# Kernel optimization log

Hardware: AMD Instinct MI355X
Metric: run time of the kernel (lower is better)

The kernel has to match this reference:

```python
import jax, jax.numpy as jnp
import numpy as np

N, V, NF, EF, EMB, OUT, MP = 512, 40, 32, 4, 128, 128, 3
BIG_NEG = -1.0e6


def _build_graph():
    """Build a batch of random molecule-like graphs (path + extra edges, one-hot
    bond features) and replicate the torch index-construction logic in numpy."""
    rng = np.random.default_rng(0)
    edges = np.zeros((N, V, V, EF), np.float32)
    perm = np.argsort(rng.random((N, V)), axis=1)
    b = np.repeat(np.arange(N), V - 1)
    i = perm[:, :-1].ravel(); j = perm[:, 1:].ravel()
    t = rng.integers(0, EF, b.shape)
    edges[b, i, j, t] = 1.0; edges[b, j, i, t] = 1.0
    NEX = 6  # extra edges per graph
    u = rng.integers(0, V, (N, NEX))
    v = rng.integers(0, V - 1, (N, NEX)); v = v + (v >= u)  # no self loops
    b2 = np.repeat(np.arange(N), NEX); t2 = rng.integers(0, EF, b2.shape)
    edges[b2, u.ravel(), v.ravel(), t2] = 1.0; edges[b2, v.ravel(), u.ravel(), t2] = 1.0
    # keep edge features strictly one-hot (adjacency = edges.sum(-1) must be 0/1)
    multi = edges.sum(-1) > 1
    edges = np.where(multi[..., None], np.eye(EF, dtype=np.float32)[edges.argmax(-1)], edges)

    adj = (edges.sum(-1) > 0).astype(np.float32)            # (N,V,V) binary
    b_idx, n_idx, nb_idx = np.nonzero(adj)                  # directed edge list, row-major
    E = b_idx.shape[0]
    adj_e = np.zeros((N, V, V), np.int64)
    adj_e[b_idx, n_idx, nb_idx] = np.arange(1, E + 1)       # edge-id+1 in adjacency slots
    rows = adj_e[b_idx, nb_idx, :]                          # (E,V): edges into each edge's nghb
    deg = (rows > 0).sum(1)
    eb = rows[rows > 0] - 1                                 # ingoing edge ids (row-major = torch cat order)
    igeb = np.repeat(np.arange(E), deg)                     # receiving-edge index
    ige = np.arange(deg.sum()) - np.repeat(np.cumsum(deg) - deg, deg)  # slot within receiver
    keep = n_idx[igeb] != nb_idx[eb]                        # drop the reverse edge
    eb, igeb, ige = eb[keep], igeb[keep], ige[keep]
    D = int(adj.sum(-1).max())                              # max node degree
    mask = np.zeros((E, D), np.float32); mask[igeb, ige] = 1.0
    node_mask = (adj.sum(-1) > 0).astype(np.float32)        # (N,V)
    return edges, b_idx, n_idx, nb_idx, eb, igeb, ige, mask, node_mask


def setup_inputs() -> dict:
    edges, b_idx, n_idx, nb_idx, eb, igeb, ige, mask, node_mask = _build_graph()
    key = jax.random.key(0)
    ks = jax.random.split(key, 8)
    def lin(k, fi, fo):
        return (jax.random.normal(k, (fi, fo), jnp.float32) / np.sqrt(fi)).astype(jnp.float32)
    return dict(
        nodes=jax.random.normal(ks[0], (N, V, NF), jnp.float32),
        edges=jnp.asarray(edges),
        W_pre=lin(ks[1], 2 * NF + EF, EMB), b_pre=jnp.zeros((EMB,), jnp.float32),
        W_att=lin(ks[2], 2 * EMB, EMB), b_att=jnp.zeros((EMB,), jnp.float32),
        W_emb=lin(ks[3], 2 * EMB, EMB), b_emb=jnp.zeros((EMB,), jnp.float32),
        Wg_att=lin(ks[4], 2 * EMB, EMB), bg_att=jnp.zeros((EMB,), jnp.float32),
        Wg_emb=lin(ks[5], EMB, EMB), bg_emb=jnp.zeros((EMB,), jnp.float32),
        W_out=lin(ks[6], EMB, OUT), b_out=jnp.zeros((OUT,), jnp.float32),
        ingoing_mask=jnp.asarray(mask), node_mask=jnp.asarray(node_mask),
        eb_b=jnp.asarray(b_idx, jnp.int32), eb_n=jnp.asarray(n_idx, jnp.int32),
        eb_nb=jnp.asarray(nb_idx, jnp.int32),
        in_eb=jnp.asarray(eb, jnp.int32), in_igeb=jnp.asarray(igeb, jnp.int32),
        in_ige=jnp.asarray(ige, jnp.int32),
    )


def reference(nodes, edges, W_pre, b_pre, W_att, b_att, W_emb, b_emb,
              Wg_att, bg_att, Wg_emb, bg_emb, W_out, b_out,
              ingoing_mask, node_mask, eb_b, eb_n, eb_nb, in_eb, in_igeb, in_ige):
    E, D = ingoing_mask.shape
    # preprocess_edges (EMN): tanh MLP on [node, neighbour, edge] per directed edge
    e_in = jnp.concatenate([nodes[eb_b, eb_n], nodes[eb_b, eb_nb],
                            edges[eb_b, eb_n, eb_nb]], axis=-1)        # (E, 2NF+EF)
    e_emb = jnp.tanh(e_in @ W_pre + b_pre)                              # (E, EMB)
    energy_mask = (1.0 - ingoing_mask)[:, :, None] * BIG_NEG            # (E, D, 1)
    e_bcast = jnp.broadcast_to(e_emb[:, None, :], (E, D, EMB))

    def step(mem, _):
        # scatter ingoing edge memories into padded (E, D, EMB) slots, then
        # attention-aggregate (propagate_edges of EMN)
        in_mem = jnp.zeros((E, D, EMB), mem.dtype).at[in_igeb, in_ige].set(mem[in_eb])
        cat = jnp.concatenate([e_bcast, in_mem], axis=-1)               # (E, D, 2EMB)
        att = jax.nn.softmax(cat @ W_att + b_att + energy_mask, axis=1)
        msg = jnp.tanh(cat @ W_emb + b_emb)
        return (att * msg).sum(1), None

    mem0 = jnp.zeros((E, EMB), nodes.dtype)
    mem, _ = jax.lax.scan(step, mem0, None, length=MP)                  # (E, EMB)
    # node_sets scatter + sum over degree slots == segment-sum per (graph, node)
    graph_sets = jax.ops.segment_sum(mem, eb_b * V + eb_n,
                                     num_segments=N * V).reshape(N, V, EMB)
    # readout: attention GraphGather + dense head
    cat3 = jnp.concatenate([graph_sets, graph_sets], axis=-1)           # hidden == input
    g_att = jax.nn.softmax(cat3 @ Wg_att + bg_att +
                           (1.0 - node_mask)[:, :, None] * BIG_NEG, axis=1)
    g_emb = jnp.tanh(graph_sets @ Wg_emb + bg_emb)
    graph_embedding = (g_att * g_emb).sum(1)                            # (N, EMB)
    return graph_embedding @ W_out + b_out                              # (N, OUT)
```

## Files before the change

### kernel.cpp

```cpp
#include <hip/hip_runtime.h>
#include <hip/hip_bf16.h>
#include <math.h>

#define NN 512
#define VN 40
#define NF 32
#define EFD 4
#define OUTD 128
#define EMAX 96
#define DMAX 8
#define MSTR 136
#define WPSTR 104
#define NT 1024
#define NW 16

typedef __attribute__((ext_vector_type(8))) short short8;
typedef __attribute__((ext_vector_type(4))) float f32x4;

__device__ __forceinline__ float fast_tanh(float x) {
    return fmaf(-2.0f, __builtin_amdgcn_rcpf(__expf(2.0f * x) + 1.0f), 1.0f);
}

__global__ __launch_bounds__(256) void k_setup(
    const int* __restrict__ igeb, const int* __restrict__ eb_b,
    const float* __restrict__ W_att, const float* __restrict__ W_emb,
    const float* __restrict__ Wg_att, const float* __restrict__ Wg_emb,
    const float* __restrict__ W_pre,
    int* __restrict__ off, int* __restrict__ eoff,
    __hip_bfloat16* __restrict__ Wt1, __hip_bfloat16* __restrict__ Wt2,
    __hip_bfloat16* __restrict__ Wt3, __hip_bfloat16* __restrict__ Wpt,
    int K, int E, int nbO, int nbK)
{
    int bid = blockIdx.x, tid = threadIdx.x;
    if (bid < nbO) {
        int e = bid * 256 + tid;
        if (e >= E) return;
        int b = eb_b[e];
        if (e == 0) { for (int bb = 0; bb <= b; ++bb) off[bb] = 0; }
        else { int pb = eb_b[e - 1]; for (int bb = pb + 1; bb <= b; ++bb) off[bb] = e; }
        if (e == E - 1) { for (int bb = b + 1; bb <= NN; ++bb) off[bb] = E; }
        return;
    }
    bid -= nbO;
    if (bid < nbK) {
        int k = bid * 256 + tid;
        if (k >= K) return;
        int e = igeb[k];
        if (k == 0) { for (int ee = 0; ee <= e; ++ee) eoff[ee] = 0; }
        else { int pe = igeb[k - 1]; for (int ee = pe + 1; ee <= e; ++ee) eoff[ee] = k; }
        if (k == K - 1) { for (int ee = e + 1; ee <= E; ++ee) eoff[ee] = K; }
        return;
    }
    bid -= nbK;
    int c = bid * 2 + (tid >> 7), k = tid & 127;
    int cc = c & 127; bool hi = c >= 128;
    if (!hi) {
        Wt1[c * 128 + k] = __float2bfloat16(W_emb[k * 128 + c]);
        if (k < WPSTR)
            Wpt[c * WPSTR + k] = __float2bfloat16(k < 68 ? W_pre[k * 128 + c] : 0.f);
    }
    Wt2[c * 128 + k] = __float2bfloat16(hi ? W_emb[(128 + k) * 128 + cc] : W_att[(128 + k) * 128 + cc]);
    Wt3[c * 128 + k] = __float2bfloat16(hi ? Wg_emb[k * 128 + cc]
                                           : (Wg_att[k * 128 + cc] + Wg_att[(128 + k) * 128 + cc]));
}

__global__ __launch_bounds__(256) void k_pre2(
    const float* __restrict__ nodes, const float* __restrict__ edges,
    const __hip_bfloat16* __restrict__ Wpt, const float* __restrict__ b_pre,
    const int* __restrict__ eb_b, const int* __restrict__ eb_n, const int* __restrict__ eb_nb,
    const __hip_bfloat16* __restrict__ Wt1, const float* __restrict__ b_emb,
    __hip_bfloat16* __restrict__ beB, int E)
{
    __shared__ __align__(16) __hip_bfloat16 eIn[64 * WPSTR];
    __shared__ __align__(16) __hip_bfloat16 eL[64 * MSTR];
    __shared__ int bL[64], nL[64], nbL[64];
    int tid = threadIdx.x;
    int e0 = blockIdx.x * 64;
    if (tid < 64) {
        int e = e0 + tid;
        int b = -1, n = 0, nb = 0;
        if (e < E) { b = eb_b[e]; n = eb_n[e]; nb = eb_nb[e]; }
        bL[tid] = b; nL[tid] = n; nbL[tid] = nb;
        float4 ev = make_float4(0.f, 0.f, 0.f, 0.f);
        if (b >= 0) ev = *(const float4*)&edges[(((size_t)b * VN + n) * VN + nb) * EFD];
        eIn[tid * WPSTR + 64] = __float2bfloat16(ev.x);
        eIn[tid * WPSTR + 65] = __float2bfloat16(ev.y);
        eIn[tid * WPSTR + 66] = __float2bfloat16(ev.z);
        eIn[tid * WPSTR + 67] = __float2bfloat16(ev.w);
        for (int f = 68; f < WPSTR; ++f) eIn[tid * WPSTR + f] = __float2bfloat16(0.f);
    }
    __syncthreads();
    #pragma unroll
    for (int it = 0; it < 4; ++it) {
        int slot = tid + it * 256;
        int le = slot >> 4, seg = slot & 15;
        int b = bL[le];
        float4 v = make_float4(0.f, 0.f, 0.f, 0.f);
        if (b >= 0) {
            int node = (seg < 8) ? nL[le] : nbL[le];
            v = *(const float4*)&nodes[((size_t)b * VN + node) * NF + (seg & 7) * 4];
        }
        __hip_bfloat16* dst = &eIn[le * WPSTR + ((seg < 8) ? 0 : 32) + (seg & 7) * 4];
        dst[0] = __float2bfloat16(v.x);
        dst[1] = __float2bfloat16(v.y);
        dst[2] = __float2bfloat16(v.z);
        dst[3] = __float2bfloat16(v.w);
    }
    __syncthreads();
    int wave = tid >> 6, lane = tid & 63, lm = lane & 15, lq = lane >> 4;
    int r0 = wave * 16;
    {
        short8 Af[3];
        #pragma unroll
        for (int kb = 0; kb < 3; ++kb)
            Af[kb] = *(const short8*)((const short*)eIn + (r0 + lm) * WPSTR + kb * 32 + lq * 8);
        #pragma unroll
        for (int t = 0; t < 8; ++t) {
            short8 Bf[3];
            #pragma unroll
            for (int kb = 0; kb < 3; ++kb)
                Bf[kb] = *(const short8*)((const short*)Wpt +
                         (size_t)(t * 16 + lm) * WPSTR + kb * 32 + lq * 8);
            f32x4 acc = {0.f, 0.f, 0.f, 0.f};
            #pragma unroll
            for (int kb = 0; kb < 3; ++kb)
                acc = __builtin_amdgcn_mfma_f32_16x16x32_bf16(Af[kb], Bf[kb], acc, 0, 0, 0);
            int col = t * 16 + lm;
            float bp = b_pre[col];
            #pragma unroll
            for (int i = 0; i < 4; ++i)
                eL[(r0 + lq * 4 + i) * MSTR + col] = __float2bfloat16(fast_tanh(acc[i] + bp));
        }
    }
    __syncthreads();
    {
        short8 Af[4];
        #pragma unroll
        for (int kb = 0; kb < 4; ++kb)
            Af[kb] = *(const short8*)((const short*)eL + (r0 + lm) * MSTR + kb * 32 + lq * 8);
        #pragma unroll
        for (int t = 0; t < 8; ++t) {
            short8 Bf[4];
            #pragma unroll
            for (int kb = 0; kb < 4; ++kb)
                Bf[kb] = *(const short8*)((const short*)Wt1 +
                         (size_t)(t * 16 + lm) * 128 + kb * 32 + lq * 8);
            f32x4 acc = {0.f, 0.f, 0.f, 0.f};
            #pragma unroll
            for (int kb = 0; kb < 4; ++kb)
                acc = __builtin_amdgcn_mfma_f32_16x16x32_bf16(Af[kb], Bf[kb], acc, 0, 0, 0);
            int col = t * 16 + lm;
            float bv = b_emb[col];
            #pragma unroll
            for (int i = 0; i < 4; ++i)
                beB[(size_t)(e0 + r0 + lq * 4 + i) * 128 + col] =
                    __float2bfloat16(__expf(2.f * (acc[i] + bv)));
        }
    }
}

__global__ __launch_bounds__(NT, 8) void k_mp(
    const __hip_bfloat16* __restrict__ beB,
    const __hip_bfloat16* __restrict__ Wt2, const __hip_bfloat16* __restrict__ Wt3,
    const float* __restrict__ bg_att, const float* __restrict__ bg_emb,
    const int* __restrict__ igeb, const int* __restrict__ ige, const int* __restrict__ ieb,
    const int* __restrict__ eoff,
    const int* __restrict__ eb_n, const float* __restrict__ node_mask,
    const float* __restrict__ W_out, const float* __restrict__ b_out,
    const int* __restrict__ off, float* __restrict__ out)
{
    __shared__ __align__(16) char pool[75264];
    __shared__ float gembL[128];
    __shared__ float nmL[VN];
    __shared__ int srcL[EMAX * DMAX];
    __shared__ int nodeL[EMAX];
    __hip_bfloat16* memL  = (__hip_bfloat16*)pool;
    unsigned*       MaMeL = (unsigned*)(pool + 26112);
    float*          nsF   = (float*)pool;
    __hip_bfloat16* nsbL  = (__hip_bfloat16*)(pool + 26112);
    unsigned*       GOLp  = (unsigned*)(pool + 39168);
    float*          numP  = (float*)pool;
    float*          denP  = (float*)(pool + 4096);
    float*          redL  = (float*)(pool + 8192);

    int b = blockIdx.x;
    int s0 = off[b], s1 = off[b + 1];
    int nE = s1 - s0;
    int tid = threadIdx.x;
    int wave = tid >> 6, lane = tid & 63, lm = lane & 15, lq = lane >> 4;

    for (int idx = tid; idx < EMAX * DMAX; idx += NT) srcL[idx] = -1;
    if (tid < EMAX) nodeL[tid] = (tid < nE) ? eb_n[s0 + tid] : 0;
    if (tid < VN) nmL[tid] = node_mask[b * VN + tid];
    __syncthreads();
    {
        int k0 = eoff[s0], k1 = eoff[s1];
        for (int k = k0 + tid; k < k1; k += NT)
            srcL[(igeb[k] - s0) * DMAX + ige[k]] = ieb[k] - s0;
    }

    for (int idx = tid; idx < EMAX * 128; idx += NT) {
        int le = idx >> 7, c = idx & 127;
        float v = 0.f;
        if (le < nE) {
            float e2be = __bfloat162float(beB[(size_t)(s0 + le) * 128 + c]);
            v = fmaf(-2.f, __builtin_amdgcn_rcpf(e2be + 1.f), 1.f);
        }
        memL[le * MSTR + c] = __float2bfloat16(v);
    }
    __syncthreads();

    for (int step = 0; step < 2; ++step) {
        for (int t = wave; t < 96; t += NW) {
            int r = t >> 4;
            int col0 = (t & 15) * 16;
            short8 Af[4], Bg[4];
            #pragma unroll
            for (int kb = 0; kb < 4; ++kb) {
                Af[kb] = *(const short8*)((const short*)memL + (r * 16 + lm) * MSTR + kb * 32 + lq * 8);
                Bg[kb] = *(const short8*)((const short*)Wt2 + (size_t)(col0 + lm) * 128 + kb * 32 + lq * 8);
            }
            f32x4 acc = {0.f, 0.f, 0.f, 0.f};
            #pragma unroll
            for (int kb = 0; kb < 4; ++kb)
                acc = __builtin_amdgcn_mfma_f32_16x16x32_bf16(Af[kb], Bg[kb], acc, 0, 0, 0);
            int col = col0 + lm;
            int cc = col & 127;
            __hip_bfloat16* hp = (__hip_bfloat16*)MaMeL;
            if (col < 128) {
                #pragma unroll
                for (int i2 = 0; i2 < 4; ++i2)
                    hp[((r * 16 + lq * 4 + i2) * 128 + cc) * 2] =
                        __float2bfloat16(__expf(acc[i2]));
            } else {
                #pragma unroll
                for (int i2 = 0; i2 < 4; ++i2)
                    hp[((r * 16 + lq * 4 + i2) * 128 + cc) * 2 + 1] =
                        __float2bfloat16(__expf(2.f * acc[i2]));
            }
        }
        __syncthreads();
        if (step == 1) {
            for (int idx = tid; idx < VN * 128; idx += NT) nsF[idx] = 0.f;
            __syncthreads();
        }
        for (int le = wave; le < nE; le += NW) {
            int sv = srcL[le * DMAX + (lane & 7)];
            float e2b0 = __bfloat162float(beB[(size_t)(s0 + le) * 128 + lane]);
            float e2b1 = __bfloat162float(beB[(size_t)(s0 + le) * 128 + 64 + lane]);
            float sw0 = 0.f, swr0 = 0.f, sw1 = 0.f, swr1 = 0.f;
            bool anyV = false;
            #pragma unroll
            for (int d = 0; d < DMAX; ++d) {
                int ls = __builtin_amdgcn_readlane(sv, d);
                if (ls >= 0) {
                    anyV = true;
                    unsigned pk0 = MaMeL[ls * 128 + lane];
                    unsigned pk1 = MaMeL[ls * 128 + 64 + lane];
                    float w0 = __uint_as_float(pk0 << 16);
                    float m0 = __uint_as_float(pk0 & 0xFFFF0000u);
                    float w1 = __uint_as_float(pk1 << 16);
                    float m1 = __uint_as_float(pk1 & 0xFFFF0000u);
                    sw0 += w0;
                    swr0 = fmaf(w0, __builtin_amdgcn_rcpf(fmaf(e2b0, m0, 1.f)), swr0);
                    sw1 += w1;
                    swr1 = fmaf(w1, __builtin_amdgcn_rcpf(fmaf(e2b1, m1, 1.f)), swr1);
                }
            }
            float r0 = anyV ? swr0 * __builtin_amdgcn_rcpf(sw0)
                            : __builtin_amdgcn_rcpf(e2b0 + 1.f);
            float r1 = anyV ? swr1 * __builtin_amdgcn_rcpf(sw1)
                            : __builtin_amdgcn_rcpf(e2b1 + 1.f);
            float v0 = fmaf(-2.f, r0, 1.f);
            float v1 = fmaf(-2.f, r1, 1.f);
            if (step == 0) {
                memL[le * MSTR + lane] = __float2bfloat16(v0);
                memL[le * MSTR + 64 + lane] = __float2bfloat16(v1);
            } else {
                int v = __builtin_amdgcn_readfirstlane(nodeL[le]);
                atomicAdd(&nsF[v * 128 + lane], v0);
                atomicAdd(&nsF[v * 128 + 64 + lane], v1);
            }
        }
        __syncthreads();
    }

    for (int idx = tid; idx < 48 * 128; idx += NT) {
        int v = idx >> 7, k = idx & 127;
        nsbL[v * MSTR + k] = __float2bfloat16(v < VN ? nsF[idx] : 0.f);
    }
    __syncthreads();
    for (int t = wave; t < 48; t += NW) {
        int r = t >> 4;
        int col0 = (t & 15) * 16;
        short8 Af[4], Bg[4];
        #pragma unroll
        for (int kb = 0; kb < 4; ++kb) {
            Af[kb] = *(const short8*)((const short*)nsbL + (r * 16 + lm) * MSTR + kb * 32 + lq * 8);
            Bg[kb] = *(const short8*)((const short*)Wt3 + (size_t)(col0 + lm) * 128 + kb * 32 + lq * 8);
        }
        f32x4 acc = {0.f, 0.f, 0.f, 0.f};
        #pragma unroll
        for (int kb = 0; kb < 4; ++kb)
            acc = __builtin_amdgcn_mfma_f32_16x16x32_bf16(Af[kb], Bg[kb], acc, 0, 0, 0);
        int col = col0 + lm;
        int cc = col & 127;
        float bv = (col < 128) ? bg_att[col] : bg_emb[cc];
        __hip_bfloat16* hp = (__hip_bfloat16*)GOLp;
        if (col < 128) {
            #pragma unroll
            for (int i2 = 0; i2 < 4; ++i2)
                hp[((r * 16 + lq * 4 + i2) * 128 + cc) * 2] =
                    __float2bfloat16(__expf(acc[i2] + bv));
        } else {
            #pragma unroll
            for (int i2 = 0; i2 < 4; ++i2)
                hp[((r * 16 + lq * 4 + i2) * 128 + cc) * 2 + 1] =
                    __float2bfloat16(__expf(2.f * (acc[i2] + bv)));
        }
    }
    __syncthreads();
    {
        int c = tid & 127, q = tid >> 7;
        float sw = 0.f, swr = 0.f;
        for (int v = q; v < VN; v += 8) {
            if (nmL[v] == 0.f) continue;
            unsigned pk = GOLp[v * 128 + c];
            float w = __uint_as_float(pk << 16);
            float e2 = __uint_as_float(pk & 0xFFFF0000u);
            sw += w;
            swr = fmaf(w, __builtin_amdgcn_rcpf(e2 + 1.f), swr);
        }
        numP[tid] = swr;
        denP[tid] = sw;
    }
    __syncthreads();
    if (tid < 128) {
        float swr = 0.f, sw = 0.f;
        #pragma unroll
        for (int p = 0; p < 8; ++p) { swr += numP[p * 128 + tid]; sw += denP[p * 128 + tid]; }
        gembL[tid] = fmaf(-2.f, swr / sw, 1.f);
    }
    __syncthreads();
    {
        int c = tid & 127, h = tid >> 7;
        float acc = 0.f;
        for (int j = h; j < 128; j += 8)
            acc += gembL[j] * W_out[j * OUTD + c];
        redL[tid] = acc;
    }
    __syncthreads();
    if (tid < 128) {
        float acc = b_out[tid];
        #pragma unroll
        for (int p = 0; p < 8; ++p) acc += redL[p * 128 + tid];
        out[(size_t)b * OUTD + tid] = acc;
    }
}

extern "C" void kernel_launch(void* const* d_in, const int* in_sizes, int n_in,
                              void* d_out, int out_size, void* d_ws, size_t ws_size,
                              hipStream_t stream) {
    const float* nodes    = (const float*)d_in[0];
    const float* edges    = (const float*)d_in[1];
    const float* W_pre    = (const float*)d_in[2];
    const float* b_pre    = (const float*)d_in[3];
    const float* W_att    = (const float*)d_in[4];
    const float* W_emb    = (const float*)d_in[6];
    const float* b_emb    = (const float*)d_in[7];
    const float* Wg_att   = (const float*)d_in[8];
    const float* bg_att   = (const float*)d_in[9];
    const float* Wg_emb   = (const float*)d_in[10];
    const float* bg_emb   = (const float*)d_in[11];
    const float* W_out    = (const float*)d_in[12];
    const float* b_out    = (const float*)d_in[13];
    const float* node_mask = (const float*)d_in[15];
    const int* eb_b   = (const int*)d_in[16];
    const int* eb_n   = (const int*)d_in[17];
    const int* eb_nb  = (const int*)d_in[18];
    const int* in_eb  = (const int*)d_in[19];
    const int* in_igeb = (const int*)d_in[20];
    const int* in_ige  = (const int*)d_in[21];

    int E = in_sizes[16];
    int K = in_sizes[19];
    int E64 = (E + 63) & ~63;

    __hip_bfloat16* Wt1 = (__hip_bfloat16*)d_ws;
    __hip_bfloat16* Wt2 = Wt1 + 128 * 128;
    __hip_bfloat16* Wt3 = Wt2 + 256 * 128;
    __hip_bfloat16* Wpt = Wt3 + 256 * 128;
    __hip_bfloat16* beB = Wpt + 128 * WPSTR;
    int* off  = (int*)(beB + (size_t)(E64 + 128) * 128);
    int* eoff = off + (NN + 1);

    int nbO = (E + 255) / 256;
    int nbK = (K + 255) / 256;

    k_setup<<<nbO + nbK + 128, 256, 0, stream>>>(in_igeb, eb_b,
                                                 W_att, W_emb, Wg_att, Wg_emb, W_pre,
                                                 off, eoff, Wt1, Wt2, Wt3, Wpt,
                                                 K, E, nbO, nbK);
    k_pre2<<<E64 / 64, 256, 0, stream>>>(nodes, edges, Wpt, b_pre,
                                         eb_b, eb_n, eb_nb, Wt1, b_emb, beB, E);
    k_mp<<<NN, NT, 0, stream>>>(beB, Wt2, Wt3, bg_att, bg_emb,
                                in_igeb, in_ige, in_eb, eoff, eb_n, node_mask,
                                W_out, b_out, off, (float*)d_out);
}
```

Before: 187.8 us.

## Fuse edge preprocessing into message-passing kernel and compact neighbor lists

Folds the k_pre2 edge-embedding GEMMs into the per-graph k_mp kernel, so each block computes its own edges' pre and emb projections in shared memory. This removes a kernel launch and the global beB round trip. It also builds compact per-edge source lists with atomic degree counters so the aggregation loops only over real neighbours, and keeps the exp(2*be) values packed in registers across steps. The att/emb GEMM tiles are now paired so each MaMe entry is written as one packed 32-bit store. The cost is more work and shared-memory traffic per block inside the already large k_mp, and the neighbour order inside srcL is no longer fixed.

```diff
diff --git a/kernel.cpp b/kernel.cpp
--- a/kernel.cpp
+++ b/kernel.cpp
@@ -19,6 +19,12 @@
 
 __device__ __forceinline__ float fast_tanh(float x) {
     return fmaf(-2.0f, __builtin_amdgcn_rcpf(__expf(2.0f * x) + 1.0f), 1.0f);
+}
+__device__ __forceinline__ unsigned bf16b(float x) {
+    __hip_bfloat16 h = __float2bfloat16(x);
+    unsigned short u;
+    __builtin_memcpy(&u, &h, 2);
+    return (unsigned)u;
 }
 
 __global__ __launch_bounds__(256) void k_setup(
@@ -64,108 +70,16 @@
                                            : (Wg_att[k * 128 + cc] + Wg_att[(128 + k) * 128 + cc]));
 }
 
-__global__ __launch_bounds__(256) void k_pre2(
+__global__ __launch_bounds__(NT, 8) void k_mp(
     const float* __restrict__ nodes, const float* __restrict__ edges,
     const __hip_bfloat16* __restrict__ Wpt, const float* __restrict__ b_pre,
-    const int* __restrict__ eb_b, const int* __restrict__ eb_n, const int* __restrict__ eb_nb,
     const __hip_bfloat16* __restrict__ Wt1, const float* __restrict__ b_emb,
-    __hip_bfloat16* __restrict__ beB, int E)
-{
-    __shared__ __align__(16) __hip_bfloat16 eIn[64 * WPSTR];
-    __shared__ __align__(16) __hip_bfloat16 eL[64 * MSTR];
-    __shared__ int bL[64], nL[64], nbL[64];
-    int tid = threadIdx.x;
-    int e0 = blockIdx.x * 64;
-    if (tid < 64) {
-        int e = e0 + tid;
-        int b = -1, n = 0, nb = 0;
-        if (e < E) { b = eb_b[e]; n = eb_n[e]; nb = eb_nb[e]; }
-        bL[tid] = b; nL[tid] = n; nbL[tid] = nb;
-        float4 ev = make_float4(0.f, 0.f, 0.f, 0.f);
-        if (b >= 0) ev = *(const float4*)&edges[(((size_t)b * VN + n) * VN + nb) * EFD];
-        eIn[tid * WPSTR + 64] = __float2bfloat16(ev.x);
-        eIn[tid * WPSTR + 65] = __float2bfloat16(ev.y);
-        eIn[tid * WPSTR + 66] = __float2bfloat16(ev.z);
-        eIn[tid * WPSTR + 67] = __float2bfloat16(ev.w);
-        for (int f = 68; f < WPSTR; ++f) eIn[tid * WPSTR + f] = __float2bfloat16(0.f);
-    }
-    __syncthreads();
-    #pragma unroll
-    for (int it = 0; it < 4; ++it) {
-        int slot = tid + it * 256;
-        int le = slot >> 4, seg = slot & 15;
-        int b = bL[le];
-        float4 v = make_float4(0.f, 0.f, 0.f, 0.f);
-        if (b >= 0) {
-            int node = (seg < 8) ? nL[le] : nbL[le];
-            v = *(const float4*)&nodes[((size_t)b * VN + node) * NF + (seg & 7) * 4];
-        }
-        __hip_bfloat16* dst = &eIn[le * WPSTR + ((seg < 8) ? 0 : 32) + (seg & 7) * 4];
-        dst[0] = __float2bfloat16(v.x);
-        dst[1] = __float2bfloat16(v.y);
-        dst[2] = __float2bfloat16(v.z);
-        dst[3] = __float2bfloat16(v.w);
-    }
-    __syncthreads();
-    int wave = tid >> 6, lane = tid & 63, lm = lane & 15, lq = lane >> 4;
-    int r0 = wave * 16;
-    {
-        short8 Af[3];
-        #pragma unroll
-        for (int kb = 0; kb < 3; ++kb)
-            Af[kb] = *(const short8*)((const short*)eIn + (r0 + lm) * WPSTR + kb * 32 + lq * 8);
-        #pragma unroll
-        for (int t = 0; t < 8; ++t) {
-            short8 Bf[3];
-            #pragma unroll
-            for (int kb = 0; kb < 3; ++kb)
-                Bf[kb] = *(const short8*)((const short*)Wpt +
-                         (size_t)(t * 16 + lm) * WPSTR + kb * 32 + lq * 8);
-            f32x4 acc = {0.f, 0.f, 0.f, 0.f};
-            #pragma unroll
-            for (int kb = 0; kb < 3; ++kb)
-                acc = __builtin_amdgcn_mfma_f32_16x16x32_bf16(Af[kb], Bf[kb], acc, 0, 0, 0);
-            int col = t * 16 + lm;
-            float bp = b_pre[col];
-            #pragma unroll
-            for (int i = 0; i < 4; ++i)
-                eL[(r0 + lq * 4 + i) * MSTR + col] = __float2bfloat16(fast_tanh(acc[i] + bp));
-        }
-    }
-    __syncthreads();
-    {
-        short8 Af[4];
-        #pragma unroll
-        for (int kb = 0; kb < 4; ++kb)
-            Af[kb] = *(const short8*)((const short*)eL + (r0 + lm) * MSTR + kb * 32 + lq * 8);
-        #pragma unroll
-        for (int t = 0; t < 8; ++t) {
-            short8 Bf[4];
-            #pragma unroll
-            for (int kb = 0; kb < 4; ++kb)
-                Bf[kb] = *(const short8*)((const short*)Wt1 +
-                         (size_t)(t * 16 + lm) * 128 + kb * 32 + lq * 8);
-            f32x4 acc = {0.f, 0.f, 0.f, 0.f};
-            #pragma unroll
-            for (int kb = 0; kb < 4; ++kb)
-                acc = __builtin_amdgcn_mfma_f32_16x16x32_bf16(Af[kb], Bf[kb], acc, 0, 0, 0);
-            int col = t * 16 + lm;
-            float bv = b_emb[col];
-            #pragma unroll
-            for (int i = 0; i < 4; ++i)
-                beB[(size_t)(e0 + r0 + lq * 4 + i) * 128 + col] =
-                    __float2bfloat16(__expf(2.f * (acc[i] + bv)));
-        }
-    }
-}
-
-__global__ __launch_bounds__(NT, 8) void k_mp(
-    const __hip_bfloat16* __restrict__ beB,
     const __hip_bfloat16* __restrict__ Wt2, const __hip_bfloat16* __restrict__ Wt3,
     const float* __restrict__ bg_att, const float* __restrict__ bg_emb,
-    const int* __restrict__ igeb, const int* __restrict__ ige, const int* __restrict__ ieb,
+    const int* __restrict__ igeb, const int* __restrict__ ieb,
     const int* __restrict__ eoff,
-    const int* __restrict__ eb_n, const float* __restrict__ node_mask,
+    const int* __restrict__ eb_n, const int* __restrict__ eb_nb,
+    const float* __restrict__ node_mask,
     const float* __restrict__ W_out, const float* __restrict__ b_out,
     const int* __restrict__ off, float* __restrict__ out)
 {
@@ -173,8 +87,14 @@
     __shared__ float gembL[128];
     __shared__ float nmL[VN];
     __shared__ int srcL[EMAX * DMAX];
+    __shared__ int degL[EMAX];
     __shared__ int nodeL[EMAX];
-    __hip_bfloat16* memL  = (__hip_bfloat16*)pool;
+    __shared__ int nbL[EMAX];
+    __hip_bfloat16* eIn  = (__hip_bfloat16*)(pool + 26112);
+    __hip_bfloat16* eL   = (__hip_bfloat16*)pool;
+    __hip_bfloat16* beL  = (__hip_bfloat16*)(pool + 26112);
+    const unsigned short* beLu = (const unsigned short*)(pool + 26112);
+    __hip_bfloat16* memL = (__hip_bfloat16*)pool;
     unsigned*       MaMeL = (unsigned*)(pool + 26112);
     float*          nsF   = (float*)pool;
     __hip_bfloat16* nsbL  = (__hip_bfloat16*)(pool + 26112);
@@ -189,72 +109,145 @@
     int tid = threadIdx.x;
     int wave = tid >> 6, lane = tid & 63, lm = lane & 15, lq = lane >> 4;
 
-    for (int idx = tid; idx < EMAX * DMAX; idx += NT) srcL[idx] = -1;
-    if (tid < EMAX) nodeL[tid] = (tid < nE) ? eb_n[s0 + tid] : 0;
+    if (tid < EMAX) {
+        degL[tid] = 0;
+        bool vld = tid < nE;
+        int n = 0, nb = 0;
+        if (vld) { n = eb_n[s0 + tid]; nb = eb_nb[s0 + tid]; }
+        nodeL[tid] = n; nbL[tid] = nb;
+        float4 ev = make_float4(0.f, 0.f, 0.f, 0.f);
+        if (vld) ev = *(const float4*)&edges[(((size_t)b * VN + n) * VN + nb) * EFD];
+        __hip_bfloat16* dst = &eIn[tid * WPSTR + 64];
+        dst[0] = __float2bfloat16(ev.x);
+        dst[1] = __float2bfloat16(ev.y);
+        dst[2] = __float2bfloat16(ev.z);
+        dst[3] = __float2bfloat16(ev.w);
+        for (int f = 68; f < 96; ++f) eIn[tid * WPSTR + f] = __float2bfloat16(0.f);
+    }
     if (tid < VN) nmL[tid] = node_mask[b * VN + tid];
     __syncthreads();
+    for (int idx = tid; idx < EMAX * 16; idx += NT) {
+        int le = idx >> 4, seg = idx & 15;
+        float4 v4 = make_float4(0.f, 0.f, 0.f, 0.f);
+        if (le < nE) {
+            int node = (seg < 8) ? nodeL[le] : nbL[le];
+            v4 = *(const float4*)&nodes[((size_t)b * VN + node) * NF + (seg & 7) * 4];
+        }
+        __hip_bfloat16* dst = &eIn[le * WPSTR + ((seg < 8) ? 0 : 32) + (seg & 7) * 4];
+        dst[0] = __float2bfloat16(v4.x);
+        dst[1] = __float2bfloat16(v4.y);
+        dst[2] = __float2bfloat16(v4.z);
+        dst[3] = __float2bfloat16(v4.w);
+    }
     {
         int k0 = eoff[s0], k1 = eoff[s1];
-        for (int k = k0 + tid; k < k1; k += NT)
-            srcL[(igeb[k] - s0) * DMAX + ige[k]] = ieb[k] - s0;
-    }
-
+        for (int k = k0 + tid; k < k1; k += NT) {
+            int le = igeb[k] - s0;
+            int pos = atomicAdd(&degL[le], 1);
+            srcL[le * DMAX + pos] = ieb[k] - s0;
+        }
+    }
+    __syncthreads();
+    for (int t = wave; t < 48; t += NW) {
+        int r = t >> 3, c = t & 7;
+        short8 Af[3], Bf[3];
+        #pragma unroll
+        for (int kb = 0; kb < 3; ++kb) {
+            Af[kb] = *(const short8*)((const short*)eIn + (r * 16 + lm) * WPSTR + kb * 32 + lq * 8);
+            Bf[kb] = *(const short8*)((const short*)Wpt + (size_t)(c * 16 + lm) * WPSTR + kb * 32 + lq * 8);
+        }
+        f32x4 acc = {0.f, 0.f, 0.f, 0.f};
+        #pragma unroll
+        for (int kb = 0; kb < 3; ++kb)
+            acc = __builtin_amdgcn_mfma_f32_16x16x32_bf16(Af[kb], Bf[kb], acc, 0, 0, 0);
+        int col = c * 16 + lm;
+        float bp = b_pre[col];
+        #pragma unroll
+        for (int i = 0; i < 4; ++i)
+            eL[(r * 16 + lq * 4 + i) * MSTR + col] = __float2bfloat16(fast_tanh(acc[i] + bp));
+    }
+    __syncthreads();
+    for (int t = wave; t < 48; t += NW) {
+        int r = t >> 3, c = t & 7;
+        short8 Af[4], Bf[4];
+        #pragma unroll
+        for (int kb = 0; kb < 4; ++kb) {
+            Af[kb] = *(const short8*)((const short*)eL + (r * 16 + lm) * MSTR + kb * 32 + lq * 8);
+            Bf[kb] = *(const short8*)((const short*)Wt1 + (size_t)(c * 16 + lm) * 128 + kb * 32 + lq * 8);
+        }
+        f32x4 acc = {0.f, 0.f, 0.f, 0.f};
+        #pragma unroll
+        for (int kb = 0; kb < 4; ++kb)
+            acc = __builtin_amdgcn_mfma_f32_16x16x32_bf16(Af[kb], Bf[kb], acc, 0, 0, 0);
+        int col = c * 16 + lm;
+        float bv = b_emb[col];
+        #pragma unroll
+        for (int i = 0; i < 4; ++i)
+            beL[(r * 16 + lq * 4 + i) * 128 + col] = __float2bfloat16(__expf(2.f * (acc[i] + bv)));
+    }
+    __syncthreads();
+    unsigned e2bP[6];
+    #pragma unroll
+    for (int i = 0; i < 6; ++i) {
+        int le = wave + i * NW;
+        unsigned lo = beLu[le * 128 + lane];
+        unsigned hi = beLu[le * 128 + 64 + lane];
+        e2bP[i] = (hi << 16) | lo;
+    }
     for (int idx = tid; idx < EMAX * 128; idx += NT) {
         int le = idx >> 7, c = idx & 127;
         float v = 0.f;
         if (le < nE) {
-            float e2be = __bfloat162float(beB[(size_t)(s0 + le) * 128 + c]);
-            v = fmaf(-2.f, __builtin_amdgcn_rcpf(e2be + 1.f), 1.f);
+            float e2 = __uint_as_float(((unsigned)beLu[idx]) << 16);
+            v = fmaf(-2.f, __builtin_amdgcn_rcpf(e2 + 1.f), 1.f);
         }
         memL[le * MSTR + c] = __float2bfloat16(v);
     }
     __syncthreads();
 
     for (int step = 0; step < 2; ++step) {
-        for (int t = wave; t < 96; t += NW) {
-            int r = t >> 4;
-            int col0 = (t & 15) * 16;
-            short8 Af[4], Bg[4];
+        for (int p = wave; p < 48; p += NW) {
+            int r = p >> 3, c = p & 7;
+            short8 Af[4], Bf[4];
             #pragma unroll
             for (int kb = 0; kb < 4; ++kb) {
                 Af[kb] = *(const short8*)((const short*)memL + (r * 16 + lm) * MSTR + kb * 32 + lq * 8);
-                Bg[kb] = *(const short8*)((const short*)Wt2 + (size_t)(col0 + lm) * 128 + kb * 32 + lq * 8);
+                Bf[kb] = *(const short8*)((const short*)Wt2 + (size_t)(c * 16 + lm) * 128 + kb * 32 + lq * 8);
             }
-            f32x4 acc = {0.f, 0.f, 0.f, 0.f};
+            f32x4 aa = {0.f, 0.f, 0.f, 0.f};
             #pragma unroll
             for (int kb = 0; kb < 4; ++kb)
-                acc = __builtin_amdgcn_mfma_f32_16x16x32_bf16(Af[kb], Bg[kb], acc, 0, 0, 0);
-            int col = col0 + lm;
-            int cc = col & 127;
-            __hip_bfloat16* hp = (__hip_bfloat16*)MaMeL;
-            if (col < 128) {
-                #pragma unroll
-                for (int i2 = 0; i2 < 4; ++i2)
-                    hp[((r * 16 + lq * 4 + i2) * 128 + cc) * 2] =
-                        __float2bfloat16(__expf(acc[i2]));
-            } else {
-                #pragma unroll
-                for (int i2 = 0; i2 < 4; ++i2)
-                    hp[((r * 16 + lq * 4 + i2) * 128 + cc) * 2 + 1] =
-                        __float2bfloat16(__expf(2.f * acc[i2]));
-            }
+                aa = __builtin_amdgcn_mfma_f32_16x16x32_bf16(Af[kb], Bf[kb], aa, 0, 0, 0);
+            #pragma unroll
+            for (int kb = 0; kb < 4; ++kb)
+                Bf[kb] = *(const short8*)((const short*)Wt2 + (size_t)(128 + c * 16 + lm) * 128 + kb * 32 + lq * 8);
+            f32x4 ae = {0.f, 0.f, 0.f, 0.f};
+            #pragma unroll
+            for (int kb = 0; kb < 4; ++kb)
+                ae = __builtin_amdgcn_mfma_f32_16x16x32_bf16(Af[kb], Bf[kb], ae, 0, 0, 0);
+            int col = c * 16 + lm, row0 = r * 16 + lq * 4;
+            #pragma unroll
+            for (int i = 0; i < 4; ++i)
+                MaMeL[(row0 + i) * 128 + col] =
+                    (bf16b(__expf(2.f * ae[i])) << 16) | bf16b(__expf(aa[i]));
         }
         __syncthreads();
         if (step == 1) {
             for (int idx = tid; idx < VN * 128; idx += NT) nsF[idx] = 0.f;
             __syncthreads();
         }
-        for (int le = wave; le < nE; le += NW) {
-            int sv = srcL[le * DMAX + (lane & 7)];
-            float e2b0 = __bfloat162float(beB[(size_t)(s0 + le) * 128 + lane]);
-            float e2b1 = __bfloat162float(beB[(size_t)(s0 + le) * 128 + 64 + lane]);
-            float sw0 = 0.f, swr0 = 0.f, sw1 = 0.f, swr1 = 0.f;
-            bool anyV = false;
-            #pragma unroll
-            for (int d = 0; d < DMAX; ++d) {
-                int ls = __builtin_amdgcn_readlane(sv, d);
-                if (ls >= 0) {
-                    anyV = true;
+        #pragma unroll
+        for (int i = 0; i < 6; ++i) {
+            int le = wave + i * NW;
+            if (le < nE) {
+                int deg = __builtin_amdgcn_readfirstlane(degL[le]);
+                int sv = srcL[le * DMAX + (lane & 7)];
+                unsigned pkb = e2bP[i];
+                float e2b0 = __uint_as_float(pkb << 16);
+                float e2b1 = __uint_as_float(pkb & 0xFFFF0000u);
+                float sw0 = 0.f, swr0 = 0.f, sw1 = 0.f, swr1 = 0.f;
+                for (int d = 0; d < deg; ++d) {
+                    int ls = __builtin_amdgcn_readlane(sv, d);
                     unsigned pk0 = MaMeL[ls * 128 + lane];
                     unsigned pk1 = MaMeL[ls * 128 + 64 + lane];
                     float w0 = __uint_as_float(pk0 << 16);
@@ -266,20 +259,20 @@
                     sw1 += w1;
                     swr1 = fmaf(w1, __builtin_amdgcn_rcpf(fmaf(e2b1, m1, 1.f)), swr1);
                 }
-            }
-            float r0 = anyV ? swr0 * __builtin_amdgcn_rcpf(sw0)
-                            : __builtin_amdgcn_rcpf(e2b0 + 1.f);
-            float r1 = anyV ? swr1 * __builtin_amdgcn_rcpf(sw1)
-                            : __builtin_amdgcn_rcpf(e2b1 + 1.f);
-            float v0 = fmaf(-2.f, r0, 1.f);
-            float v1 = fmaf(-2.f, r1, 1.f);
-            if (step == 0) {
-                memL[le * MSTR + lane] = __float2bfloat16(v0);
-                memL[le * MSTR + 64 + lane] = __float2bfloat16(v1);
-            } else {
-                int v = __builtin_amdgcn_readfirstlane(nodeL[le]);
-                atomicAdd(&nsF[v * 128 + lane], v0);
-                atomicAdd(&nsF[v * 128 + 64 + lane], v1);
+                float r0 = deg ? swr0 * __builtin_amdgcn_rcpf(sw0)
+                               : __builtin_amdgcn_rcpf(e2b0 + 1.f);
+                float r1 = deg ? swr1 * __builtin_amdgcn_rcpf(sw1)
+                               : __builtin_amdgcn_rcpf(e2b1 + 1.f);
+                float v0 = fmaf(-2.f, r0, 1.f);
+                float v1 = fmaf(-2.f, r1, 1.f);
+                if (step == 0) {
+                    memL[le * MSTR + lane] = __float2bfloat16(v0);
+                    memL[le * MSTR + 64 + lane] = __float2bfloat16(v1);
+                } else {
+                    int v = __builtin_amdgcn_readfirstlane(nodeL[le]);
+                    atomicAdd(&nsF[v * 128 + lane], v0);
+                    atomicAdd(&nsF[v * 128 + 64 + lane], v1);
+                }
             }
         }
         __syncthreads();
@@ -380,18 +373,15 @@
     const int* eb_nb  = (const int*)d_in[18];
     const int* in_eb  = (const int*)d_in[19];
     const int* in_igeb = (const int*)d_in[20];
-    const int* in_ige  = (const int*)d_in[21];
 
     int E = in_sizes[16];
     int K = in_sizes[19];
-    int E64 = (E + 63) & ~63;
 
     __hip_bfloat16* Wt1 = (__hip_bfloat16*)d_ws;
     __hip_bfloat16* Wt2 = Wt1 + 128 * 128;
     __hip_bfloat16* Wt3 = Wt2 + 256 * 128;
     __hip_bfloat16* Wpt = Wt3 + 256 * 128;
-    __hip_bfloat16* beB = Wpt + 128 * WPSTR;
-    int* off  = (int*)(beB + (size_t)(E64 + 128) * 128);
+    int* off  = (int*)(Wpt + 128 * WPSTR);
     int* eoff = off + (NN + 1);
 
     int nbO = (E + 255) / 256;
@@ -401,9 +391,8 @@
                                                  W_att, W_emb, Wg_att, Wg_emb, W_pre,
                                                  off, eoff, Wt1, Wt2, Wt3, Wpt,
                                                  K, E, nbO, nbK);
-    k_pre2<<<E64 / 64, 256, 0, stream>>>(nodes, edges, Wpt, b_pre,
-                                         eb_b, eb_n, eb_nb, Wt1, b_emb, beB, E);
-    k_mp<<<NN, NT, 0, stream>>>(beB, Wt2, Wt3, bg_att, bg_emb,
-                                in_igeb, in_ige, in_eb, eoff, eb_n, node_mask,
+    k_mp<<<NN, NT, 0, stream>>>(nodes, edges, Wpt, b_pre, Wt1, b_emb,
+                                Wt2, Wt3, bg_att, bg_emb,
+                                in_igeb, in_eb, eoff, eb_n, eb_nb, node_mask,
                                 W_out, b_out, off, (float*)d_out);
 }
```

New measurement: 181.2 us. 1.04x faster.
